# Performance work log

Hardware: AMD Instinct MI355X
Metric: run time of the kernel (lower is better)

The kernel has to match this reference:

```python
import jax, jax.numpy as jnp
import numpy as np

N_QUBITS = 8
REPS = 2
DIM = 2 ** N_QUBITS  # 256
C64 = jnp.complex64


def _apply_1q(state, gate, wire):
    """Apply a single-qubit gate. state: [B]+[2]*n, gate: [2,2] or [B,2,2]."""
    s = jnp.moveaxis(state, wire + 1, -1)
    if gate.ndim == 2:
        s = jnp.einsum('ij,b...j->b...i', gate, s)
    else:
        s = jnp.einsum('bij,b...j->b...i', gate, s)
    return jnp.moveaxis(s, -1, wire + 1)


def _cnot(state, ctrl, tgt):
    """CNOT: flip target axis where control bit == 1. state: [B]+[2]*n."""
    s0 = jax.lax.index_in_dim(state, 0, ctrl + 1, keepdims=True)
    s1 = jax.lax.index_in_dim(state, 1, ctrl + 1, keepdims=True)
    s1 = jnp.flip(s1, axis=tgt + 1)
    return jnp.concatenate([s0, s1], axis=ctrl + 1)


def _rx(a):
    """Batched RX gate. a: [B] -> [B,2,2] complex64."""
    c = jnp.cos(0.5 * a).astype(C64)
    s = jnp.sin(0.5 * a).astype(C64)
    mis = (-1j) * s
    return jnp.stack([jnp.stack([c, mis], -1), jnp.stack([mis, c], -1)], -2)


def _rot(phi, theta, omega):
    """PennyLane Rot = RZ(omega) RY(theta) RZ(phi). Scalars -> [2,2] complex64."""
    c = jnp.cos(0.5 * theta).astype(C64)
    s = jnp.sin(0.5 * theta).astype(C64)
    ep = jnp.exp(-0.5j * (phi + omega).astype(C64))   # e^{-i(phi+omega)/2}
    em = jnp.exp(-0.5j * (phi - omega).astype(C64))   # e^{-i(phi-omega)/2}
    epc = jnp.exp(0.5j * (phi + omega).astype(C64))
    emc = jnp.exp(0.5j * (phi - omega).astype(C64))
    return jnp.stack([
        jnp.stack([ep * c, -emc * s], -1),
        jnp.stack([em * s, epc * c], -1),
    ], -2)


def _circuit(x, theta):
    B = x.shape[0]
    state = jnp.zeros((B, DIM), C64).at[:, 0].set(1.0)
    state = state.reshape((B,) + (2,) * N_QUBITS)
    # AngleEmbedding (default rotation='X'): RX(x[:, w]) on wire w
    for w in range(N_QUBITS):
        state = _apply_1q(state, _rx(x[:, w]), w)
    # StronglyEntanglingLayers: per layer, Rot on every wire then ring of CNOTs
    for l in range(REPS):
        for w in range(N_QUBITS):
            g = _rot(theta[l, w, 0], theta[l, w, 1], theta[l, w, 2])
            state = _apply_1q(state, g, w)
        r = (l % (N_QUBITS - 1)) + 1  # PennyLane default ranges
        for w in range(N_QUBITS):
            state = _cnot(state, w, (w + r) % N_QUBITS)
    # expval(PauliZ(0)): wire 0 is the most significant axis
    probs = (state.real ** 2 + state.imag ** 2).reshape(B, 2, DIM // 2)
    ev = probs[:, 0].sum(-1) - probs[:, 1].sum(-1)
    return ((ev + 1.0) * 0.5)[:, None]  # [B, 1]


def setup_inputs() -> dict:
    key = jax.random.key(0)
    kx, kt = jax.random.split(key)
    x = jax.random.normal(kx, (131072, N_QUBITS), dtype=jnp.float32)
    theta = 0.1 * jax.random.normal(kt, (REPS, N_QUBITS, 3), dtype=jnp.float32)
    return {"x": x, "theta": theta}


def reference(x, theta):
    return _circuit(x, theta)
```

## Files before the change

### kernel.cpp

```cpp
#include <hip/hip_runtime.h>


typedef _Float16 v8hf __attribute__((ext_vector_type(8)));
typedef float v4f __attribute__((ext_vector_type(4)));

#define MAGIC 0x13572468

struct cpx { float re, im; };
__device__ __forceinline__ cpx cmul(cpx a, cpx b) {
    return {a.re * b.re - a.im * b.im, a.re * b.im + a.im * b.re};
}

__device__ __forceinline__ cpx pget(int a, int i, int j) {
    static const float RE[4][4] = {{1, 0, 0, 1}, {0, 1, 1, 0},
                                   {0, 0, 0, 0}, {1, 0, 0, -1}};
    static const float IM[4][4] = {{0, 0, 0, 0}, {0, 0, 0, 0},
                                   {0, -1, 1, 0}, {0, 0, 0, 0}};
    cpx r; r.re = RE[a][i * 2 + j]; r.im = IM[a][i * 2 + j];
    return r;
}

__device__ float ptm_entry(const float* __restrict__ theta, int g, int a, int b) {
    const int l = g >> 3, w = g & 7;
    const float phi = theta[(l * 8 + w) * 3 + 0];
    const float th  = theta[(l * 8 + w) * 3 + 1];
    const float om  = theta[(l * 8 + w) * 3 + 2];
    const float c = cosf(0.5f * th), s = sinf(0.5f * th);
    const float ps = 0.5f * (phi + om), ms = 0.5f * (phi - om);
    cpx G[2][2];
    G[0][0] = {c * cosf(ps), -c * sinf(ps)};
    G[0][1] = {-s * cosf(ms), -s * sinf(ms)};
    G[1][0] = {s * cosf(ms), -s * sinf(ms)};
    G[1][1] = {c * cosf(ps), c * sinf(ps)};
    cpx M1[2][2], H[2][2];
#pragma unroll
    for (int i = 0; i < 2; ++i)
#pragma unroll
        for (int j = 0; j < 2; ++j) {
            cpx acc{0.f, 0.f};
#pragma unroll
            for (int k = 0; k < 2; ++k) {
                cpx t = cmul(pget(a, i, k), G[k][j]);
                acc.re += t.re; acc.im += t.im;
            }
            M1[i][j] = acc;
        }
#pragma unroll
    for (int i = 0; i < 2; ++i)
#pragma unroll
        for (int j = 0; j < 2; ++j) {
            cpx acc{0.f, 0.f};
#pragma unroll
            for (int k = 0; k < 2; ++k) {
                cpx gc{G[k][i].re, -G[k][i].im};
                cpx t = cmul(gc, M1[k][j]);
                acc.re += t.re; acc.im += t.im;
            }
            H[i][j] = acc;
        }
    float tr = 0.f;
#pragma unroll
    for (int i = 0; i < 2; ++i)
#pragma unroll
        for (int j = 0; j < 2; ++j) {
            cpx pb = pget(b, i, j);
            tr += pb.re * H[j][i].re - pb.im * H[j][i].im;
        }
    return 0.5f * tr;
}

__device__ void cnot_entry(int pr, int cand, int* CIDX, float* CSGN) {
    const int pc = pr >> 2, pt = pr & 3;
    const int a = cand >> 2, b2 = cand & 3;
    const int perm[4] = {0, 1, 3, 2};
    float ov = 0.f;
#pragma unroll
    for (int r = 0; r < 4; ++r)
#pragma unroll
        for (int c2 = 0; c2 < 4; ++c2) {
            const int rp = perm[r], cp = perm[c2];
            cpx Rv = cmul(pget(pc, rp >> 1, cp >> 1), pget(pt, rp & 1, cp & 1));
            cpx Kv = cmul(pget(a, r >> 1, c2 >> 1), pget(b2, r & 1, c2 & 1));
            ov += Kv.re * Rv.re + Kv.im * Rv.im;
        }
    ov *= 0.25f;
    if (ov > 0.5f) { CIDX[pr] = cand; CSGN[pr] = 1.f; }
    else if (ov < -0.5f) { CIDX[pr] = cand; CSGN[pr] = -1.f; }
}

#define OFF_AF   0
#define OFF_R    6912
#define OFF_FLAG (6912 + 16 * 729)
#define WS_FLOATS_NEEDED (OFF_FLAG + 16)

__device__ __forceinline__ int ring_conj(int cur, int r, const int* CIDX,
                                         const float* CSGN, float& sg) {
    for (int w = 7; w >= 0; --w) {
        const int tw = (w + r) & 7;
        const int pc = (cur >> (2 * w)) & 3;
        const int pt = (cur >> (2 * tw)) & 3;
        const int q = pc * 4 + pt;
        const int nq = CIDX[q];
        sg *= CSGN[q];
        cur = (cur & ~((3 << (2 * w)) | (3 << (2 * tw))))
            | ((nq >> 2) << (2 * w)) | ((nq & 3) << (2 * tw));
    }
    return cur;
}

template <int SLP>
__device__ __forceinline__ void spin_on(int* p) {
    while (__hip_atomic_load(p, __ATOMIC_ACQUIRE, __HIP_MEMORY_SCOPE_AGENT)
           != MAGIC) {
        __builtin_amdgcn_s_sleep(SLP);
    }
}

__global__ __launch_bounds__(1024) void k_prep2(const float* __restrict__ theta,
                                                float* __restrict__ ws) {
    __shared__ float SH[8780];
    __shared__ int   S1k, S1n;
    __shared__ float S1sgn;
    __shared__ int   S1w[8], S1l[8];

    const int tid = threadIdx.x;
    const int blk = blockIdx.x;
    float* Rg = ws + OFF_R;
    int*   FL = (int*)(ws + OFF_FLAG);

    if (blk < 16) {
        float* TR   = SH;
        float* CSGN = SH + 256;
        int*   CIDX = (int*)(SH + 272);
        float* Wa   = SH + 288;
        float* Wb   = SH + 4384;
        const int sa0 = blk >> 2, sa1 = blk & 3;

        if (tid < 256) TR[tid] = ptm_entry(theta, tid >> 4, (tid >> 2) & 3, tid & 3);
        else if (tid < 512) {
            const int r = tid - 256;
            cnot_entry(r >> 4, r & 15, CIDX, CSGN);
        }
        for (int i = tid; i < 4096; i += 1024) Wa[i] = 0.f;
        __syncthreads();

        if (tid == 0) {
            float sg = 1.f;
            int cur = ring_conj(3 , 2, CIDX, CSGN, sg);
            int k = 0;
            for (int w = 0; w < 8; ++w) {
                const int ltr = (cur >> (2 * w)) & 3;
                if (ltr != 0) { S1w[k] = w; S1l[k] = ltr; ++k; }
            }
            int n = 1;
            for (int i = 0; i < k; ++i) n *= 3;
            S1sgn = sg; S1k = k; S1n = n;
        }
        __syncthreads();
        const int k1 = S1k, n1 = S1n;

        for (int t = tid; t < n1; t += 1024) {
            float c = S1sgn;
            int s = 0;
            int tt = t;
            for (int i = 0; i < k1; ++i) {
                const int bl = tt % 3 + 1;
                tt /= 3;
                c *= TR[(8 + S1w[i]) * 16 + S1l[i] * 4 + bl];
                s |= bl << (2 * S1w[i]);
            }
            float sg = 1.f;
            s = ring_conj(s, 1, CIDX, CSGN, sg);
            c *= sg;
            if (((s & 3) == sa0) && (((s >> 2) & 3) == sa1)) {
                int d4 = 0;
#pragma unroll
                for (int w = 2; w < 8; ++w)
                    d4 |= ((s >> (2 * w)) & 3) << (2 * (7 - w));
                Wa[d4] = c;
            }
        }
        __syncthreads();

        const int P3c[6] = {1, 3, 9, 27, 81, 243};
        const int N4c[6] = {1024, 256, 64, 16, 4, 1};
#pragma unroll
        for (int tl = 0; tl < 6; ++tl) {
            const int w = 7 - tl;
            const float* src = (tl & 1) ? Wb : Wa;
            float* dst = (tl & 1) ? Wa : Wb;
            const int p3 = P3c[tl];
            const int Nout = p3 * 3 * N4c[tl];
            for (int idx = tid; idx < Nout; idx += 1024) {
                const int q3 = idx % p3;
                const int rest = idx / p3;
                const int P = rest % 3;
                const int r = rest / 3;
                const int let = (P == 0) ? 0 : ((P == 1) ? 3 : 2);
                const float* ib = src + q3 + p3 * 4 * r;
                dst[idx] = ib[0] * TR[w * 16 + 0 + let]
                         + ib[p3] * TR[w * 16 + 4 + let]
                         + ib[2 * p3] * TR[w * 16 + 8 + let]
                         + ib[3 * p3] * TR[w * 16 + 12 + let];
            }
            __syncthreads();
        }
        for (int k = tid; k < 729; k += 1024)
            __hip_atomic_store(&Rg[blk * 729 + k], Wa[k],
                               __ATOMIC_RELAXED, __HIP_MEMORY_SCOPE_AGENT);
        __syncthreads();
        if (tid == 0)
            __hip_atomic_store(&FL[blk], MAGIC,
                               __ATOMIC_RELEASE, __HIP_MEMORY_SCOPE_AGENT);
    } else {
        float* BIG = SH;
        float* TRw = SH + 8748;
        if (tid < 32)
            TRw[tid] = ptm_entry(theta, tid >> 4, (tid >> 2) & 3, tid & 3);
        if (tid < 16) spin_on<2>(&FL[tid]);
        __syncthreads();

        for (int idx1 = tid; idx1 < 8748; idx1 += 1024) {
            const int a0 = idx1 / 2187;
            const int rem = idx1 % 2187;
            const int P1 = rem / 729;
            const int qq = rem % 729;
            const int let = (P1 == 0) ? 0 : ((P1 == 1) ? 3 : 2);
            float v = 0.f;
#pragma unroll
            for (int a1 = 0; a1 < 4; ++a1)
                v += __hip_atomic_load(&Rg[(a0 * 4 + a1) * 729 + qq],
                                       __ATOMIC_RELAXED, __HIP_MEMORY_SCOPE_AGENT)
                     * TRw[16 + a1 * 4 + let];
            BIG[idx1] = v;
        }
        __syncthreads();

        int* AFi = (int*)(ws + OFF_AF);
        for (int u = tid; u < 6912; u += 1024) {
            const int t = u >> 8;
            const int rem = u & 255;
            const int lane = rem >> 2;
            const int jj0 = (rem & 3) * 2;
            const int m = lane & 15;
            const int q0 = m >> 2, s0 = m & 3;
            const int jb = (lane >> 4) * 8;
            unsigned int packed = 0;
#pragma unroll
            for (int z = 0; z < 2; ++z) {
                const int j = jb + jj0 + z;
                float v = 0.f;
                if (q0 < 3 && s0 < 3 && j < 27) {
                    const int i = q0 * 81 + s0 * 27 + t;
                    const int idxF = i * 27 + j;
                    const int P0 = idxF / 2187;
                    const int rest2 = idxF % 2187;
                    const int let = (P0 == 0) ? 0 : ((P0 == 1) ? 3 : 2);
                    v = BIG[rest2] * TRw[0 + let]
                      + BIG[2187 + rest2] * TRw[4 + let]
                      + BIG[2 * 2187 + rest2] * TRw[8 + let]
                      + BIG[3 * 2187 + rest2] * TRw[12 + let];
                }
                const _Float16 hv = (_Float16)v;
                const unsigned short bits = __builtin_bit_cast(unsigned short, hv);
                packed |= ((unsigned int)bits) << (16 * z);
            }
            AFi[u] = (int)packed;
        }
    }
}

__global__ __launch_bounds__(256) void k_main6(const float* __restrict__ x,
                                               const int* __restrict__ wsAF,
                                               float* __restrict__ out,
                                               int ngroups) {
    __shared__ int AFl[6912];
    const int tid = threadIdx.x;
    for (int u = tid; u < 6912; u += 256) AFl[u] = wsAF[u];
    __syncthreads();

    const int lane = tid & 63;
    const int q = lane >> 4, e = lane & 15;
    const v8hf* AFp = (const v8hf*)AFl;
    const int wave = blockIdx.x * 4 + (tid >> 6);
    const bool q0b = (q == 0), q1b = (q == 1), q2b = (q == 2);

    for (int gi = 0; gi < 4; ++gi) {
        const int g = wave * 4 + gi;
        if (g >= ngroups) break;
        const int b = g * 16 + e;
        const float4* xp = (const float4*)(x + (size_t)b * 8);
        const float4 xa = xp[0], xb = xp[1];

        float cw[8], msw[8];
        {
            const float xs[8] = {xa.x, xa.y, xa.z, xa.w, xb.x, xb.y, xb.z, xb.w};
#pragma unroll
            for (int w = 0; w < 8; ++w) {
                float sv, cv;
                __sincosf(xs[w], &sv, &cv);
                cw[w] = cv;
                msw[w] = -sv;
            }
        }

        float F2[27];
        {
            const float m5v[3] = {1.f, cw[5], msw[5]};
            const float m6v[3] = {1.f, cw[6], msw[6]};
            const float m7v[3] = {1.f, cw[7], msw[7]};
#pragma unroll
            for (int a = 0; a < 3; ++a)
#pragma unroll
                for (int b2 = 0; b2 < 3; ++b2) {
                    const float p = m5v[a] * m6v[b2];
#pragma unroll
                    for (int c2 = 0; c2 < 3; ++c2)
                        F2[(a * 3 + b2) * 3 + c2] = p * m7v[c2];
                }
        }
        v8hf bf;
#pragma unroll
        for (int jj = 0; jj < 8; ++jj) {
            const float c0 = F2[jj];
            const float c1 = F2[jj + 8];
            const float c2 = F2[jj + 16];
            const float c3 = (jj < 3) ? F2[jj + 24] : 0.f;
            const float v = q0b ? c0 : (q1b ? c1 : (q2b ? c2 : c3));
            bf[jj] = (_Float16)v;
        }

        const v4f zero = {0.f, 0.f, 0.f, 0.f};
        float h[9];
#pragma unroll
        for (int t = 0; t < 27; ++t) {
            const int a = t / 9, b2 = (t / 3) % 3, c2 = t % 3;
            v4f acc = __builtin_amdgcn_mfma_f32_16x16x32_f16(
                AFp[t * 64 + lane], bf, zero, 0, 0, 0);
            float f = fmaf(cw[1], acc[1], acc[0]);
            f = fmaf(msw[1], acc[2], f);
            if (c2 == 0)      h[a * 3 + b2] = f;
            else if (c2 == 1) h[a * 3 + b2] = fmaf(cw[4], f, h[a * 3 + b2]);
            else              h[a * 3 + b2] = fmaf(msw[4], f, h[a * 3 + b2]);
        }
        float e0 = fmaf(cw[3], h[1], h[0]); e0 = fmaf(msw[3], h[2], e0);
        float e1 = fmaf(cw[3], h[4], h[3]); e1 = fmaf(msw[3], h[5], e1);
        float e2 = fmaf(cw[3], h[7], h[6]); e2 = fmaf(msw[3], h[8], e2);
        float ev = fmaf(cw[2], e1, e0);
        ev = fmaf(msw[2], e2, ev);
        const float g0 = q0b ? 1.f : (q1b ? cw[0] : (q2b ? msw[0] : 0.f));
        ev *= g0;

        ev += __shfl_xor(ev, 16, 64);
        ev += __shfl_xor(ev, 32, 64);
        if (lane < 16) out[b] = (ev + 1.f) * 0.5f;
    }
}

struct c32 { float x, y; };

__device__ __forceinline__ c32 shfl_xor_c(c32 v, int mask) {
    c32 r;
    r.x = __shfl_xor(v.x, mask, 64);
    r.y = __shfl_xor(v.y, mask, 64);
    return r;
}
__device__ __forceinline__ c32 cmadd2(c32 ga, c32 a, c32 gp, c32 p) {
    c32 n;
    n.x = ga.x * a.x - ga.y * a.y + gp.x * p.x - gp.y * p.y;
    n.y = ga.x * a.y + ga.y * a.x + gp.x * p.y + gp.y * p.x;
    return n;
}
__device__ __forceinline__ c32 rx_mix(float c, float s, c32 a, c32 p) {
    c32 n;
    n.x = c * a.x + s * p.y;
    n.y = c * a.y - s * p.x;
    return n;
}
__device__ __forceinline__ void apply_rx(c32 st[4], int lane, int bb, float c, float s) {
    if (bb < 6) {
#pragma unroll
        for (int r = 0; r < 4; ++r) {
            c32 p = shfl_xor_c(st[r], 1 << bb);
            st[r] = rx_mix(c, s, st[r], p);
        }
    } else if (bb == 6) {
        c32 n0 = rx_mix(c, s, st[0], st[1]);
        c32 n1 = rx_mix(c, s, st[1], st[0]);
        c32 n2 = rx_mix(c, s, st[2], st[3]);
        c32 n3 = rx_mix(c, s, st[3], st[2]);
        st[0] = n0; st[1] = n1; st[2] = n2; st[3] = n3;
    } else {
        c32 n0 = rx_mix(c, s, st[0], st[2]);
        c32 n2 = rx_mix(c, s, st[2], st[0]);
        c32 n1 = rx_mix(c, s, st[1], st[3]);
        c32 n3 = rx_mix(c, s, st[3], st[1]);
        st[0] = n0; st[1] = n1; st[2] = n2; st[3] = n3;
    }
}
__device__ __forceinline__ void apply_rot(c32 st[4], int lane, int bb,
                                          c32 g00, c32 g01, c32 g10, c32 g11) {
    if (bb < 6) {
#pragma unroll
        for (int r = 0; r < 4; ++r) {
            c32 p = shfl_xor_c(st[r], 1 << bb);
            bool hi = (lane >> bb) & 1;
            c32 ga, gp;
            ga.x = hi ? g11.x : g00.x;
            ga.y = hi ? g11.y : g00.y;
            gp.x = hi ? g10.x : g01.x;
            gp.y = hi ? g10.y : g01.y;
            st[r] = cmadd2(ga, st[r], gp, p);
        }
    } else if (bb == 6) {
        c32 n0 = cmadd2(g00, st[0], g01, st[1]);
        c32 n1 = cmadd2(g10, st[0], g11, st[1]);
        c32 n2 = cmadd2(g00, st[2], g01, st[3]);
        c32 n3 = cmadd2(g10, st[2], g11, st[3]);
        st[0] = n0; st[1] = n1; st[2] = n2; st[3] = n3;
    } else {
        c32 n0 = cmadd2(g00, st[0], g01, st[2]);
        c32 n2 = cmadd2(g10, st[0], g11, st[2]);
        c32 n1 = cmadd2(g00, st[1], g01, st[3]);
        c32 n3 = cmadd2(g10, st[1], g11, st[3]);
        st[0] = n0; st[1] = n1; st[2] = n2; st[3] = n3;
    }
}
__device__ __forceinline__ void cswap(bool c, c32& a, c32& b) {
    c32 t = a;
    a.x = c ? b.x : a.x; a.y = c ? b.y : a.y;
    b.x = c ? t.x : b.x; b.y = c ? t.y : b.y;
}
__device__ __forceinline__ void apply_cnot(c32 st[4], int lane, int bc, int bt) {
    if (bt < 6) {
        if (bc < 6) {
            bool ctrl = (lane >> bc) & 1;
#pragma unroll
            for (int r = 0; r < 4; ++r) {
                c32 p = shfl_xor_c(st[r], 1 << bt);
                st[r].x = ctrl ? p.x : st[r].x;
                st[r].y = ctrl ? p.y : st[r].y;
            }
        } else {
#pragma unroll
            for (int r = 0; r < 4; ++r) {
                if ((r >> (bc - 6)) & 1) st[r] = shfl_xor_c(st[r], 1 << bt);
            }
        }
    } else {
        if (bc < 6) {
            bool ctrl = (lane >> bc) & 1;
            if (bt == 6) { cswap(ctrl, st[0], st[1]); cswap(ctrl, st[2], st[3]); }
            else         { cswap(ctrl, st[0], st[2]); cswap(ctrl, st[1], st[3]); }
        } else {
            if (bc == 7 && bt == 6) { c32 t = st[2]; st[2] = st[3]; st[3] = t; }
            else if (bc == 6 && bt == 7) { c32 t = st[1]; st[1] = st[3]; st[3] = t; }
        }
    }
}
__global__ __launch_bounds__(256) void qsim_kernel(const float* __restrict__ x,
                                                   const float* __restrict__ theta,
                                                   float* __restrict__ out,
                                                   int batch) {
    __shared__ float rot[2 * 8 * 8];
    const int t = threadIdx.x;
    if (t < 16) {
        const int l = t >> 3, w = t & 7;
        const float phi = theta[(l * 8 + w) * 3 + 0];
        const float th  = theta[(l * 8 + w) * 3 + 1];
        const float om  = theta[(l * 8 + w) * 3 + 2];
        const float c = cosf(0.5f * th), s = sinf(0.5f * th);
        const float p = 0.5f * (phi + om), m = 0.5f * (phi - om);
        float* g = &rot[t * 8];
        g[0] = c * cosf(p);  g[1] = -c * sinf(p);
        g[2] = -s * cosf(m); g[3] = -s * sinf(m);
        g[4] = s * cosf(m);  g[5] = -s * sinf(m);
        g[6] = c * cosf(p);  g[7] = c * sinf(p);
    }
    __syncthreads();
    const int lane = t & 63;
    const int b = blockIdx.x * 4 + (t >> 6);
    if (b >= batch) return;
    float c8 = 0.f, s8 = 0.f;
    if (lane < 8) {
        const float xv = 0.5f * x[b * 8 + lane];
        c8 = cosf(xv); s8 = sinf(xv);
    }
    c32 st[4];
#pragma unroll
    for (int r = 0; r < 4; ++r) { st[r].x = 0.f; st[r].y = 0.f; }
    if (lane == 0) st[0].x = 1.f;
#pragma unroll
    for (int w = 0; w < 8; ++w) {
        const float c = __shfl(c8, w, 64);
        const float s = __shfl(s8, w, 64);
        apply_rx(st, lane, 7 - w, c, s);
    }
#pragma unroll
    for (int l = 0; l < 2; ++l) {
#pragma unroll
        for (int w = 0; w < 8; ++w) {
            const float* g = &rot[(l * 8 + w) * 8];
            c32 g00{g[0], g[1]}, g01{g[2], g[3]}, g10{g[4], g[5]}, g11{g[6], g[7]};
            apply_rot(st, lane, 7 - w, g00, g01, g10, g11);
        }
        const int rr = l + 1;
#pragma unroll
        for (int w = 0; w < 8; ++w) apply_cnot(st, lane, 7 - w, 7 - ((w + rr) & 7));
    }
    float v = st[0].x * st[0].x + st[0].y * st[0].y
            + st[1].x * st[1].x + st[1].y * st[1].y
            - st[2].x * st[2].x - st[2].y * st[2].y
            - st[3].x * st[3].x - st[3].y * st[3].y;
#pragma unroll
    for (int off = 32; off > 0; off >>= 1) v += __shfl_xor(v, off, 64);
    if (lane == 0) out[b] = (v + 1.f) * 0.5f;
}

extern "C" void kernel_launch(void* const* d_in, const int* in_sizes, int n_in,
                              void* d_out, int out_size, void* d_ws, size_t ws_size,
                              hipStream_t stream) {
    const float* x     = (const float*)d_in[0];
    const float* theta = (const float*)d_in[1];
    float* out = (float*)d_out;
    const int batch = in_sizes[0] / 8;

    if (ws_size >= (size_t)WS_FLOATS_NEEDED * 4 + 256 && (batch & 15) == 0) {
        float* ws = (float*)d_ws;
        k_prep2<<<dim3(17), dim3(1024), 0, stream>>>(theta, ws);
        const int ngroups = batch / 16;
        k_main6<<<dim3(512), dim3(256), 0, stream>>>(
            x, (const int*)ws + OFF_AF, out, ngroups);
    } else {
        qsim_kernel<<<dim3((batch + 3) / 4), dim3(256), 0, stream>>>(x, theta, out, batch);
    }
}
```

Measured before the change: 76.95 us.

## Fuse theta-dependent transfer-matrix prep into main kernel, recomputed per block

Removes the separate 17-block prep kernel and its global-memory flag spin handoff. Each block of the main kernel now rebuilds the fp16 MFMA operand table in LDS from theta itself, looping over 9 Pauli prefix pairs with shared atomics. It also holds the operand fragments in registers and prefetches x for 8 groups per wave. The trade is one fewer launch and no inter-block sync, against redundant prep work in all 256 blocks and higher register and LDS use.

```diff
diff --git a/kernel.cpp b/kernel.cpp
--- a/kernel.cpp
+++ b/kernel.cpp
@@ -3,8 +3,6 @@
 
 typedef _Float16 v8hf __attribute__((ext_vector_type(8)));
 typedef float v4f __attribute__((ext_vector_type(4)));
-
-#define MAGIC 0x13572468
 
 struct cpx { float re, im; };
 __device__ __forceinline__ cpx cmul(cpx a, cpx b) {
@@ -88,11 +86,6 @@
     else if (ov < -0.5f) { CIDX[pr] = cand; CSGN[pr] = -1.f; }
 }
 
-#define OFF_AF   0
-#define OFF_R    6912
-#define OFF_FLAG (6912 + 16 * 729)
-#define WS_FLOATS_NEEDED (OFF_FLAG + 16)
-
 __device__ __forceinline__ int ring_conj(int cur, int r, const int* CIDX,
                                          const float* CSGN, float& sg) {
     for (int w = 7; w >= 0; --w) {
@@ -108,76 +101,92 @@
     return cur;
 }
 
-template <int SLP>
-__device__ __forceinline__ void spin_on(int* p) {
-    while (__hip_atomic_load(p, __ATOMIC_ACQUIRE, __HIP_MEMORY_SCOPE_AGENT)
-           != MAGIC) {
-        __builtin_amdgcn_s_sleep(SLP);
-    }
-}
-
-__global__ __launch_bounds__(1024) void k_prep2(const float* __restrict__ theta,
-                                                float* __restrict__ ws) {
-    __shared__ float SH[8780];
+__global__ __launch_bounds__(256, 1) void k_one(const float* __restrict__ x,
+                                                const float* __restrict__ theta,
+                                                float* __restrict__ out,
+                                                int ngroups) {
+    __shared__ int   AFl[6912];
+    __shared__ float Wa[4096];
+    __shared__ float Wb[3072];
+    __shared__ float TR[256];
+    __shared__ float CSGN[16];
+    __shared__ int   CIDX[16];
     __shared__ int   S1k, S1n;
     __shared__ float S1sgn;
     __shared__ int   S1w[8], S1l[8];
 
     const int tid = threadIdx.x;
-    const int blk = blockIdx.x;
-    float* Rg = ws + OFF_R;
-    int*   FL = (int*)(ws + OFF_FLAG);
-
-    if (blk < 16) {
-        float* TR   = SH;
-        float* CSGN = SH + 256;
-        int*   CIDX = (int*)(SH + 272);
-        float* Wa   = SH + 288;
-        float* Wb   = SH + 4384;
-        const int sa0 = blk >> 2, sa1 = blk & 3;
-
-        if (tid < 256) TR[tid] = ptm_entry(theta, tid >> 4, (tid >> 2) & 3, tid & 3);
-        else if (tid < 512) {
-            const int r = tid - 256;
-            cnot_entry(r >> 4, r & 15, CIDX, CSGN);
-        }
-        for (int i = tid; i < 4096; i += 1024) Wa[i] = 0.f;
-        __syncthreads();
-
-        if (tid == 0) {
-            float sg = 1.f;
-            int cur = ring_conj(3 , 2, CIDX, CSGN, sg);
-            int k = 0;
-            for (int w = 0; w < 8; ++w) {
-                const int ltr = (cur >> (2 * w)) & 3;
-                if (ltr != 0) { S1w[k] = w; S1l[k] = ltr; ++k; }
-            }
-            int n = 1;
-            for (int i = 0; i < k; ++i) n *= 3;
-            S1sgn = sg; S1k = k; S1n = n;
-        }
-        __syncthreads();
-        const int k1 = S1k, n1 = S1n;
-
-        for (int t = tid; t < n1; t += 1024) {
+
+    TR[tid] = ptm_entry(theta, tid >> 4, (tid >> 2) & 3, tid & 3);
+    cnot_entry(tid >> 4, tid & 15, CIDX, CSGN);
+#pragma unroll
+    for (int u = tid; u < 6912; u += 256) AFl[u] = 0;
+    __syncthreads();
+
+    if (tid == 0) {
+        float sg = 1.f;
+        int cur = ring_conj(3 , 2, CIDX, CSGN, sg);
+        int k = 0;
+        for (int w = 0; w < 8; ++w) {
+            const int ltr = (cur >> (2 * w)) & 3;
+            if (ltr != 0) { S1w[k] = w; S1l[k] = ltr; ++k; }
+        }
+        int n = 1;
+        for (int i = 0; i < k; ++i) n *= 3;
+        S1sgn = sg; S1k = k; S1n = n;
+    }
+    __syncthreads();
+    const int k1 = S1k, n1 = S1n;
+
+    int   pk[26];
+    float cf[26];
+#pragma unroll
+    for (int i = 0; i < 26; ++i) {
+        pk[i] = -1;
+        cf[i] = 0.f;
+        const int t = tid + 256 * i;
+        if (t < n1) {
             float c = S1sgn;
             int s = 0;
             int tt = t;
-            for (int i = 0; i < k1; ++i) {
-                const int bl = tt % 3 + 1;
-                tt /= 3;
-                c *= TR[(8 + S1w[i]) * 16 + S1l[i] * 4 + bl];
-                s |= bl << (2 * S1w[i]);
+#pragma unroll
+            for (int ii = 0; ii < 8; ++ii) {
+                if (ii < k1) {
+                    const int bl = tt % 3 + 1;
+                    tt /= 3;
+                    c *= TR[(8 + S1w[ii]) * 16 + S1l[ii] * 4 + bl];
+                    s |= bl << (2 * S1w[ii]);
+                }
             }
             float sg = 1.f;
             s = ring_conj(s, 1, CIDX, CSGN, sg);
             c *= sg;
-            if (((s & 3) == sa0) && (((s >> 2) & 3) == sa1)) {
-                int d4 = 0;
-#pragma unroll
-                for (int w = 2; w < 8; ++w)
-                    d4 |= ((s >> (2 * w)) & 3) << (2 * (7 - w));
-                Wa[d4] = c;
+            const int a0 = s & 3, a1 = (s >> 2) & 3;
+            int d4 = 0;
+#pragma unroll
+            for (int w = 2; w < 8; ++w)
+                d4 |= ((s >> (2 * w)) & 3) << (2 * (7 - w));
+            pk[i] = (d4 << 4) | (a0 << 2) | a1;
+            cf[i] = c;
+        }
+    }
+
+    _Float16* AF16 = (_Float16*)AFl;
+    for (int p = 0; p < 9; ++p) {
+        const int P0 = p / 3, P1 = p % 3;
+        const int let0 = (P0 == 0) ? 0 : ((P0 == 1) ? 3 : 2);
+        const int let1 = (P1 == 0) ? 0 : ((P1 == 1) ? 3 : 2);
+
+        for (int u = tid; u < 4096; u += 256) Wa[u] = 0.f;
+        __syncthreads();
+
+#pragma unroll
+        for (int i = 0; i < 26; ++i) {
+            if (pk[i] >= 0) {
+                const int a0 = (pk[i] >> 2) & 3, a1 = pk[i] & 3;
+                const int d4 = pk[i] >> 4;
+                const float v = cf[i] * TR[a0 * 4 + let0] * TR[16 + a1 * 4 + let1];
+                atomicAdd(&Wa[d4], v);
             }
         }
         __syncthreads();
@@ -191,7 +200,7 @@
             float* dst = (tl & 1) ? Wa : Wb;
             const int p3 = P3c[tl];
             const int Nout = p3 * 3 * N4c[tl];
-            for (int idx = tid; idx < Nout; idx += 1024) {
+            for (int idx = tid; idx < Nout; idx += 256) {
                 const int q3 = idx % p3;
                 const int rest = idx / p3;
                 const int P = rest % 3;
@@ -205,100 +214,50 @@
             }
             __syncthreads();
         }
-        for (int k = tid; k < 729; k += 1024)
-            __hip_atomic_store(&Rg[blk * 729 + k], Wa[k],
-                               __ATOMIC_RELAXED, __HIP_MEMORY_SCOPE_AGENT);
+        const int m = 4 * P0 + P1;
+        for (int idx = tid; idx < 729; idx += 256) {
+            const int T = idx / 27, j = idx % 27;
+            const int h = (T * 64 + (j >> 3) * 16 + m) * 8 + (j & 7);
+            AF16[h] = (_Float16)Wa[idx];
+        }
         __syncthreads();
-        if (tid == 0)
-            __hip_atomic_store(&FL[blk], MAGIC,
-                               __ATOMIC_RELEASE, __HIP_MEMORY_SCOPE_AGENT);
-    } else {
-        float* BIG = SH;
-        float* TRw = SH + 8748;
-        if (tid < 32)
-            TRw[tid] = ptm_entry(theta, tid >> 4, (tid >> 2) & 3, tid & 3);
-        if (tid < 16) spin_on<2>(&FL[tid]);
-        __syncthreads();
-
-        for (int idx1 = tid; idx1 < 8748; idx1 += 1024) {
-            const int a0 = idx1 / 2187;
-            const int rem = idx1 % 2187;
-            const int P1 = rem / 729;
-            const int qq = rem % 729;
-            const int let = (P1 == 0) ? 0 : ((P1 == 1) ? 3 : 2);
-            float v = 0.f;
-#pragma unroll
-            for (int a1 = 0; a1 < 4; ++a1)
-                v += __hip_atomic_load(&Rg[(a0 * 4 + a1) * 729 + qq],
-                                       __ATOMIC_RELAXED, __HIP_MEMORY_SCOPE_AGENT)
-                     * TRw[16 + a1 * 4 + let];
-            BIG[idx1] = v;
-        }
-        __syncthreads();
-
-        int* AFi = (int*)(ws + OFF_AF);
-        for (int u = tid; u < 6912; u += 1024) {
-            const int t = u >> 8;
-            const int rem = u & 255;
-            const int lane = rem >> 2;
-            const int jj0 = (rem & 3) * 2;
-            const int m = lane & 15;
-            const int q0 = m >> 2, s0 = m & 3;
-            const int jb = (lane >> 4) * 8;
-            unsigned int packed = 0;
-#pragma unroll
-            for (int z = 0; z < 2; ++z) {
-                const int j = jb + jj0 + z;
-                float v = 0.f;
-                if (q0 < 3 && s0 < 3 && j < 27) {
-                    const int i = q0 * 81 + s0 * 27 + t;
-                    const int idxF = i * 27 + j;
-                    const int P0 = idxF / 2187;
-                    const int rest2 = idxF % 2187;
-                    const int let = (P0 == 0) ? 0 : ((P0 == 1) ? 3 : 2);
-                    v = BIG[rest2] * TRw[0 + let]
-                      + BIG[2187 + rest2] * TRw[4 + let]
-                      + BIG[2 * 2187 + rest2] * TRw[8 + let]
-                      + BIG[3 * 2187 + rest2] * TRw[12 + let];
-                }
-                const _Float16 hv = (_Float16)v;
-                const unsigned short bits = __builtin_bit_cast(unsigned short, hv);
-                packed |= ((unsigned int)bits) << (16 * z);
-            }
-            AFi[u] = (int)packed;
-        }
-    }
-}
-
-__global__ __launch_bounds__(256) void k_main6(const float* __restrict__ x,
-                                               const int* __restrict__ wsAF,
-                                               float* __restrict__ out,
-                                               int ngroups) {
-    __shared__ int AFl[6912];
-    const int tid = threadIdx.x;
-    for (int u = tid; u < 6912; u += 256) AFl[u] = wsAF[u];
-    __syncthreads();
+    }
 
     const int lane = tid & 63;
     const int q = lane >> 4, e = lane & 15;
+    const bool q0b = (q == 0), q1b = (q == 1), q2b = (q == 2);
     const v8hf* AFp = (const v8hf*)AFl;
+    v8hf af[27];
+#pragma unroll
+    for (int t = 0; t < 27; ++t) af[t] = AFp[t * 64 + lane];
+
     const int wave = blockIdx.x * 4 + (tid >> 6);
-    const bool q0b = (q == 0), q1b = (q == 1), q2b = (q == 2);
-
-    for (int gi = 0; gi < 4; ++gi) {
-        const int g = wave * 4 + gi;
+
+    float4 xs0[8], xs1[8];
+#pragma unroll
+    for (int gi = 0; gi < 8; ++gi) {
+        const int g = wave * 8 + gi;
+        if (g < ngroups) {
+            const float4* xp = (const float4*)(x + (size_t)(g * 16 + e) * 8);
+            xs0[gi] = xp[0];
+            xs1[gi] = xp[1];
+        }
+    }
+
+#pragma unroll 1
+    for (int gi = 0; gi < 8; ++gi) {
+        const int g = wave * 8 + gi;
         if (g >= ngroups) break;
         const int b = g * 16 + e;
-        const float4* xp = (const float4*)(x + (size_t)b * 8);
-        const float4 xa = xp[0], xb = xp[1];
+        const float4 xa = xs0[gi], xb = xs1[gi];
 
         float cw[8], msw[8];
         {
-            const float xs[8] = {xa.x, xa.y, xa.z, xa.w, xb.x, xb.y, xb.z, xb.w};
+            const float xv[8] = {xa.x, xa.y, xa.z, xa.w, xb.x, xb.y, xb.z, xb.w};
 #pragma unroll
             for (int w = 0; w < 8; ++w) {
                 float sv, cv;
-                __sincosf(xs[w], &sv, &cv);
+                __sincosf(xv[w], &sv, &cv);
                 cw[w] = cv;
                 msw[w] = -sv;
             }
@@ -313,10 +272,10 @@
             for (int a = 0; a < 3; ++a)
 #pragma unroll
                 for (int b2 = 0; b2 < 3; ++b2) {
-                    const float p = m5v[a] * m6v[b2];
+                    const float pp = m5v[a] * m6v[b2];
 #pragma unroll
                     for (int c2 = 0; c2 < 3; ++c2)
-                        F2[(a * 3 + b2) * 3 + c2] = p * m7v[c2];
+                        F2[(a * 3 + b2) * 3 + c2] = pp * m7v[c2];
                 }
         }
         v8hf bf;
@@ -335,8 +294,7 @@
 #pragma unroll
         for (int t = 0; t < 27; ++t) {
             const int a = t / 9, b2 = (t / 3) % 3, c2 = t % 3;
-            v4f acc = __builtin_amdgcn_mfma_f32_16x16x32_f16(
-                AFp[t * 64 + lane], bf, zero, 0, 0, 0);
+            v4f acc = __builtin_amdgcn_mfma_f32_16x16x32_f16(af[t], bf, zero, 0, 0, 0);
             float f = fmaf(cw[1], acc[1], acc[0]);
             f = fmaf(msw[1], acc[2], f);
             if (c2 == 0)      h[a * 3 + b2] = f;
@@ -525,12 +483,10 @@
     float* out = (float*)d_out;
     const int batch = in_sizes[0] / 8;
 
-    if (ws_size >= (size_t)WS_FLOATS_NEEDED * 4 + 256 && (batch & 15) == 0) {
-        float* ws = (float*)d_ws;
-        k_prep2<<<dim3(17), dim3(1024), 0, stream>>>(theta, ws);
+    if ((batch & 15) == 0) {
         const int ngroups = batch / 16;
-        k_main6<<<dim3(512), dim3(256), 0, stream>>>(
-            x, (const int*)ws + OFF_AF, out, ngroups);
+        const int blocks = (ngroups + 31) / 32;
+        k_one<<<dim3(blocks), dim3(256), 0, stream>>>(x, theta, out, ngroups);
     } else {
         qsim_kernel<<<dim3((batch + 3) / 4), dim3(256), 0, stream>>>(x, theta, out, batch);
     }
```

Result: slower. 129.6 us (+68.4%).
